# Optimization experiments

Measured on AMD Instinct MI355X. Metric: run time of the kernel, lower is better.

The kernel has to match this reference:

```python
import jax, jax.numpy as jnp
import numpy as np

DELTA = 0.1
LRELU_SLOPE = 0.01
BN_EPS = 1e-5


def ternarize(t, d):
    # {-1, 0, +1}: 0 where |t| < d, sign(t) otherwise (matches the torch where-chain)
    return jnp.where(jnp.abs(t) < d, 0.0, jnp.sign(t))


def ste_ternarize(t, d):
    # straight-through estimator, matching the torch .data-swap trick
    return t + jax.lax.stop_gradient(ternarize(t, d) - t)


def conv2d(x, w, stride, pad):
    return jax.lax.conv_general_dilated(
        x, w, (stride, stride), [(pad, pad), (pad, pad)],
        dimension_numbers=('NCHW', 'OIHW', 'NCHW'))


def batchnorm(x, gamma, beta, mean, var):
    inv = gamma / jnp.sqrt(var + BN_EPS)
    return x * inv[None, :, None, None] + (beta - mean * inv)[None, :, None, None]


def lrelu(x):
    return jnp.where(x > 0, x, LRELU_SLOPE * x)


def setup_inputs() -> dict:
    key = jax.random.key(0)
    ks = jax.random.split(key, 12)
    B, Cin, C, H, W = 16, 32, 64, 256, 256
    return {
        'x':      jax.random.normal(ks[0], (B, Cin, H, W), jnp.float32),
        'w11':    jax.random.normal(ks[1], (C, Cin, 3, 3), jnp.float32),
        'b11':    jax.random.normal(ks[2], (C,), jnp.float32),
        'w1':     jax.random.normal(ks[3], (C, Cin, 3, 3), jnp.float32),
        'b1':     jax.random.normal(ks[4], (C,), jnp.float32),
        'w2':     jax.random.normal(ks[5], (C, C, 3, 3), jnp.float32),
        'b2':     jax.random.normal(ks[6], (C,), jnp.float32),
        'gamma_p': jax.random.uniform(ks[7], (Cin,), jnp.float32),
        'beta_p':  jax.random.normal(ks[8], (Cin,), jnp.float32),
        'mean_p':  jax.random.normal(ks[9], (Cin,), jnp.float32),
        'var_p':   jnp.ones((Cin,), jnp.float32),
        'gamma1':  jax.random.uniform(ks[10], (C,), jnp.float32),
        'beta1':   jax.random.normal(ks[11], (C,), jnp.float32),
        'mean1':   jax.random.normal(jax.random.fold_in(key, 99), (C,), jnp.float32),
        'var1':    jnp.ones((C,), jnp.float32),
    }


def reference(x, w11, b11, w1, b1, w2, b2,
              gamma_p, beta_p, mean_p, var_p,
              gamma1, beta1, mean1, var1):
    # shortcut conv11 (stride 3); NOTE: torch mutates input.data in-place, so
    # the main branch below consumes the x already ternarized with d11.
    d11 = DELTA * jnp.max(jnp.abs(w11))
    x_t = ste_ternarize(x, d11)
    prev_mp = conv2d(x_t, ste_ternarize(w11, d11), 3, 1) \
        + ste_ternarize(b11, d11)[None, :, None, None]

    # main branch: pre_bn -> lrelu -> conv1 (stride 1) -> bn1 -> lrelu -> dropout(eval) -> conv2 (stride 3)
    out = lrelu(batchnorm(x_t, gamma_p, beta_p, mean_p, var_p))

    d1 = DELTA * jnp.max(jnp.abs(w1))
    out = conv2d(ste_ternarize(out, d1), ste_ternarize(w1, d1), 1, 1) \
        + ste_ternarize(b1, d1)[None, :, None, None]
    out = lrelu(batchnorm(out, gamma1, beta1, mean1, var1))
    # dropout: identity in eval mode

    d2 = DELTA * jnp.max(jnp.abs(w2))
    out = conv2d(ste_ternarize(out, d2), ste_ternarize(w2, d2), 3, 1) \
        + ste_ternarize(b2, d2)[None, :, None, None]

    return lrelu(out + prev_mp)  # [16, 64, 86, 86]
```

## Files before the change

### kernel.cpp

```cpp
#include <hip/hip_runtime.h>
#include <stdint.h>

#define B 16
#define CIN 32
#define C 64
#define H 256
#define W 256
#define OH 86
#define OW 86
#define PIX (OH*OW)
#define PADW 272
#define PWORDS (PADW*PADW*8)

typedef int v4i __attribute__((ext_vector_type(4)));

#define OFF_D      0
#define OFF_MAPW   64
#define OFF_B11    768
#define OFF_B2     1280
#define OFF_TLO    1536
#define OFF_THI    1792
#define OFF_W11R   4096
#define OFF_W1R    24576
#define OFF_W2R    45056
#define OFF_XTP    262144
#define OFF_XMAP   38141952

__device__ __forceinline__ int tern_i(float t, float d) {
    return (fabsf(t) < d) ? 0 : (t > 0.f ? 1 : -1);
}

__global__ __launch_bounds__(256) void k_pad(char* ws) {
    int idx = blockIdx.x * 256 + threadIdx.x;
    if (blockIdx.x == 0 && threadIdx.x < 3)
        ((unsigned*)(ws + OFF_D))[threadIdx.x] = 0u;
    if (idx >= 135168) return;
    int n = idx / 8448, c = idx - n * 8448;
    int row, col;
    if (c < 4352) {
        int r = c / 272; col = c - r * 272; row = (r < 2) ? r : r + 256;
    } else {
        int c2 = c - 4352; int k = c2 & 15;
        row = 2 + (c2 >> 4); col = (k < 2) ? k : k + 256;
    }
    size_t base = ((size_t)n * (PADW * PADW) + (size_t)row * PADW + col) * 2;
    int4 z = make_int4(0, 0, 0, 0);
    ((int4*)(ws + OFF_XTP))[base] = z;  ((int4*)(ws + OFF_XTP))[base + 1] = z;
    ((int4*)(ws + OFF_XMAP))[base] = z; ((int4*)(ws + OFF_XMAP))[base + 1] = z;
}

__global__ __launch_bounds__(256) void k_absmax(const float* w11, const float* w1,
                                                const float* w2, unsigned* dws) {
    __shared__ unsigned red[256];
    int b = blockIdx.x >> 4, sub = blockIdx.x & 15;
    const float* p = (b == 0) ? w11 : (b == 1) ? w1 : w2;
    int n = (b == 2) ? 36864 : 18432;
    int chunk = (n + 15) >> 4;
    int lo = sub * chunk, hi = min(lo + chunk, n);
    unsigned m = 0;
    for (int i = lo + threadIdx.x; i < hi; i += 256)
        m = max(m, __float_as_uint(fabsf(p[i])));
    red[threadIdx.x] = m; __syncthreads();
    for (int s = 128; s > 0; s >>= 1) {
        if (threadIdx.x < s) red[threadIdx.x] = max(red[threadIdx.x], red[threadIdx.x + s]);
        __syncthreads();
    }
    if (threadIdx.x == 0) atomicMax(&dws[b], red[0]);
}

__global__ __launch_bounds__(256) void k_prep(const float* w11, const float* w1, const float* w2,
                                              const float* b11, const float* b1, const float* b2,
                                              const float* gp, const float* bp, const float* mp, const float* vp,
                                              const float* g1, const float* be1, const float* me1, const float* v1,
                                              char* ws) {
    const unsigned* dw = (const unsigned*)(ws + OFF_D);
    float d11 = __fmul_rn(0.1f, __uint_as_float(dw[0]));
    float d1  = __fmul_rn(0.1f, __uint_as_float(dw[1]));
    float d2v = __fmul_rn(0.1f, __uint_as_float(dw[2]));
    int idx = blockIdx.x * 256 + threadIdx.x;
    if (idx < 4608) {
        int j = idx & 3, c16 = (idx >> 2) & 15, cot = (idx >> 6) & 3;
        int q1 = (idx >> 8) & 1, pos = idx >> 9;
        int co = cot * 16 + c16;
        unsigned wd = 0;
        #pragma unroll
        for (int jj = 0; jj < 4; jj++) {
            int ci = q1 * 16 + j * 4 + jj;
            int tv = tern_i(w1[(co * 32 + ci) * 9 + pos], d1);
            wd |= ((unsigned)(tv & 255)) << (8 * jj);
        }
        ((int*)(ws + OFF_W1R))[idx] = (int)wd;
    } else if (idx < 9216) {
        int i2 = idx - 4608;
        int j = i2 & 3, c16 = (i2 >> 2) & 15, cot = (i2 >> 6) & 3;
        int q1 = (i2 >> 8) & 1, pos = i2 >> 9;
        int co = cot * 16 + c16;
        unsigned wd = 0;
        #pragma unroll
        for (int jj = 0; jj < 4; jj++) {
            int ci = q1 * 16 + j * 4 + jj;
            int tv = tern_i(w11[(co * 32 + ci) * 9 + pos], d11);
            wd |= ((unsigned)(tv & 255)) << (8 * jj);
        }
        ((int*)(ws + OFF_W11R))[i2] = (int)wd;
    } else if (idx < 18432) {
        int i2 = idx - 9216;
        int j = i2 & 3, q = (i2 >> 2) & 3, c16 = (i2 >> 4) & 15;
        int cot = (i2 >> 8) & 3, pos = i2 >> 10;
        int co = cot * 16 + c16;
        unsigned wd = 0;
        #pragma unroll
        for (int jj = 0; jj < 4; jj++) {
            int ci = q * 16 + j * 4 + jj;
            int tv = tern_i(w2[(co * 64 + ci) * 9 + pos], d2v);
            wd |= ((unsigned)(tv & 255)) << (8 * jj);
        }
        ((int*)(ws + OFF_W2R))[i2] = (int)wd;
    } else {
        int i = idx - 18432;
        if (i < 64) {
            ((int*)(ws + OFF_B11))[i] = tern_i(b11[i], d11);
        } else if (i < 128) {
            ((int*)(ws + OFF_B2))[i - 64] = tern_i(b2[i - 64], d2v);
        } else if (i < 152) {
            int j = i - 128;
            int g = j / 3, s = j % 3;
            float v = (float)(s - 1);
            unsigned wd = 0;
            #pragma unroll
            for (int jj = 0; jj < 4; jj++) {
                int c = g * 4 + jj;
                float inv = __fdiv_rn(gp[c], __fsqrt_rn(__fadd_rn(vp[c], 1e-5f)));
                float sh  = __fsub_rn(bp[c], __fmul_rn(mp[c], inv));
                float z   = __fadd_rn(__fmul_rn(v, inv), sh);
                z = (z > 0.f) ? z : __fmul_rn(0.01f, z);
                wd |= ((unsigned)(tern_i(z, d1) & 255)) << (8 * jj);
            }
            ((int*)(ws + OFF_MAPW))[j] = (int)wd;
        } else if (i < 216) {
            int co = i - 152;
            float inv = __fdiv_rn(g1[co], __fsqrt_rn(__fadd_rn(v1[co], 1e-5f)));
            float sh  = __fsub_rn(be1[co], __fmul_rn(me1[co], inv));
            int lo = 1000, hi = 1000;
            for (int vi = -290; vi <= 290; ++vi) {
                float z = __fadd_rn(__fmul_rn((float)vi, inv), sh);
                z = (z > 0.f) ? z : __fmul_rn(0.01f, z);
                int cls = (fabsf(z) < d2v) ? 0 : (z > 0.f ? 1 : -1);
                if (cls >= 0 && lo == 1000) lo = vi;
                if (cls == 1 && hi == 1000) hi = vi;
            }
            int b1t = tern_i(b1[co], d1);
            ((int*)(ws + OFF_TLO))[co] = lo - b1t;
            ((int*)(ws + OFF_THI))[co] = hi - b1t;
        }
    }
}

__global__ __launch_bounds__(256) void k_tern_x(const float* __restrict__ x,
                                                char* __restrict__ ws) {
    float d11 = __fmul_rn(0.1f, __uint_as_float(((const unsigned*)(ws + OFF_D))[0]));
    const int* mapw = (const int*)(ws + OFF_MAPW);
    int idx = blockIdx.x * 256 + threadIdx.x;
    int pix = idx & 65535, n = idx >> 16;
    int y = pix >> 8, xq = pix & 255;
    const float* xp = x + ((size_t)n * CIN << 16) + pix;
    int rw[8], mw[8];
    #pragma unroll
    for (int g = 0; g < 8; ++g) {
        unsigned r = 0, m = 0;
        #pragma unroll
        for (int j = 0; j < 4; ++j) {
            float v = xp[(size_t)(g * 4 + j) << 16];
            int tv = tern_i(v, d11);
            r |= ((unsigned)(tv & 255)) << (8 * j);
            m |= (((unsigned)mapw[g * 3 + tv + 1] >> (8 * j)) & 255u) << (8 * j);
        }
        rw[g] = (int)r; mw[g] = (int)m;
    }
    size_t base = ((size_t)n * (PADW * PADW) + (size_t)(y + 2) * PADW + (xq + 2)) * 2;
    int4* o1 = (int4*)(ws + OFF_XTP) + base;
    o1[0] = make_int4(rw[0], rw[1], rw[2], rw[3]);
    o1[1] = make_int4(rw[4], rw[5], rw[6], rw[7]);
    int4* o2 = (int4*)(ws + OFF_XMAP) + base;
    o2[0] = make_int4(mw[0], mw[1], mw[2], mw[3]);
    o2[1] = make_int4(mw[4], mw[5], mw[6], mw[7]);
}

__global__ __launch_bounds__(256, 4) void k_net(const char* __restrict__ ws,
                                                float* __restrict__ out) {
    __shared__ int t2L[576 * 16];
    int tid = threadIdx.x, bid = blockIdx.x;
    int tx = bid % 11; int tt = bid / 11; int ty = tt % 11; int n = tt / 11;
    int OH0 = ty * 8, OW0 = tx * 8;
    int Y0 = OH0 * 3 - 2, X0 = OW0 * 3 - 2;
    int c16 = tid & 15, q = (tid >> 4) & 3, wv = tid >> 6;
    int q1 = q & 1, qh = q >> 1;
    const int* xmapn = (const int*)(ws + OFF_XMAP) + (size_t)n * PWORDS;
    const int* xtpn  = (const int*)(ws + OFF_XTP)  + (size_t)n * PWORDS;

    const int* w1r = (const int*)(ws + OFF_W1R);
    v4i bw1[5][4];
    #pragma unroll
    for (int c = 0; c < 5; ++c) {
        int pos = 2 * c + qh;
        #pragma unroll
        for (int ct = 0; ct < 4; ++ct) {
            v4i z = {0, 0, 0, 0};
            if (pos < 9) z = *(const v4i*)&w1r[((pos * 2 + q1) * 4 + ct) * 64 + c16 * 4];
            bw1[c][ct] = z;
        }
    }
    const int* TLO = (const int*)(ws + OFF_TLO);
    const int* THI = (const int*)(ws + OFF_THI);
    int tlo[4], thi[4];
    #pragma unroll
    for (int ct = 0; ct < 4; ++ct) { tlo[ct] = TLO[ct * 16 + c16]; thi[ct] = THI[ct * 16 + c16]; }

    int Yb = Y0 + 2, Xb = X0 + 2;
    #pragma unroll 1
    for (int pg = 0; pg < 9; ++pg) {
        int pbase = (wv * 9 + pg) * 16;
        int fp = pbase + c16;
        int iy = fp / 24, ix = fp - iy * 24;
        v4i a[5];
        #pragma unroll
        for (int c = 0; c < 5; ++c) {
            int pos = 2 * c + qh;
            v4i z = {0, 0, 0, 0};
            if (pos < 9) {
                int kh = pos / 3, kw = pos - kh * 3;
                z = *(const v4i*)&xmapn[((Yb + iy + kh) * PADW + (Xb + ix + kw)) * 8 + q1 * 4];
            }
            a[c] = z;
        }
        int pwr = pbase + q * 4 + (c16 & 3);
        int wy = pwr / 24, wx = pwr - wy * 24;
        bool wok = ((unsigned)(Y0 + 1 + wy) < H) && ((unsigned)(X0 + 1 + wx) < W);
        int wsw = (pwr >> 1) & 3;
        #pragma unroll
        for (int ct = 0; ct < 4; ++ct) {
            v4i acc = {0, 0, 0, 0};
            #pragma unroll
            for (int c = 0; c < 5; ++c)
                acc = __builtin_amdgcn_mfma_i32_16x16x64_i8(a[c], bw1[c][ct], acc, 0, 0, 0);
            unsigned wcol = 0;
            #pragma unroll
            for (int i = 0; i < 4; ++i) {
                int cls = (acc[i] >= tlo[ct] ? 1 : 0) + (acc[i] >= thi[ct] ? 1 : 0) - 1;
                wcol |= ((unsigned)(cls & 255)) << (8 * i);
            }
            unsigned y1 = (unsigned)__shfl_xor((int)wcol, 1);
            unsigned z1 = ((c16 & 1) == 0)
                        ? __builtin_amdgcn_perm(y1, wcol, 0x06020400u)
                        : __builtin_amdgcn_perm(y1, wcol, 0x03070105u);
            unsigned y2 = (unsigned)__shfl_xor((int)z1, 2);
            unsigned r  = ((c16 & 2) == 0)
                        ? __builtin_amdgcn_perm(y2, z1, 0x05040100u)
                        : __builtin_amdgcn_perm(y2, z1, 0x03020706u);
            t2L[pwr * 16 + (ct ^ wsw) * 4 + (c16 >> 2)] = wok ? (int)r : 0;
        }
    }
    __syncthreads();

    int o = wv * 16 + c16;
    int oh8 = o >> 3, ow8 = o & 7;
    int gOH = OH0 + oh8, gOW = OW0 + ow8;
    v4i a11[5];
    #pragma unroll
    for (int c = 0; c < 5; ++c) {
        int pos = 2 * c + qh;
        v4i z = {0, 0, 0, 0};
        if (pos < 9) {
            int kh = pos / 3, kw = pos - kh * 3;
            int ih = gOH * 3 - 1 + kh, iw = gOW * 3 - 1 + kw;
            z = *(const v4i*)&xtpn[((ih + 2) * PADW + (iw + 2)) * 8 + q1 * 4];
        }
        a11[c] = z;
    }
    v4i a2[9];
    #pragma unroll
    for (int pos = 0; pos < 9; ++pos) {
        int kh = pos / 3, kw = pos - kh * 3;
        int p2 = (oh8 * 3 + kh) * 24 + ow8 * 3 + kw;
        int g2 = q ^ ((p2 >> 1) & 3);
        a2[pos] = *(const v4i*)&t2L[p2 * 16 + g2 * 4];
    }
    const int* w2r = (const int*)(ws + OFF_W2R);
    const int* w11r = (const int*)(ws + OFF_W11R);
    v4i acc2[4], acc11[4];
    #pragma unroll
    for (int ct = 0; ct < 4; ++ct) {
        v4i acc = {0, 0, 0, 0};
        #pragma unroll
        for (int pos = 0; pos < 9; ++pos) {
            v4i b = *(const v4i*)&w2r[((pos * 4 + ct) * 16 + c16) * 16 + q * 4];
            acc = __builtin_amdgcn_mfma_i32_16x16x64_i8(a2[pos], b, acc, 0, 0, 0);
        }
        acc2[ct] = acc;
        v4i acc1 = {0, 0, 0, 0};
        #pragma unroll
        for (int c = 0; c < 5; ++c) {
            int pos = 2 * c + qh;
            v4i b = {0, 0, 0, 0};
            if (pos < 9) b = *(const v4i*)&w11r[((pos * 2 + q1) * 4 + ct) * 64 + c16 * 4];
            acc1 = __builtin_amdgcn_mfma_i32_16x16x64_i8(a11[c], b, acc1, 0, 0, 0);
        }
        acc11[ct] = acc1;
    }

    const int* b2i = (const int*)(ws + OFF_B2);
    const int* b11i = (const int*)(ws + OFF_B11);
    int pt0 = wv * 16 + q * 4;
    int ohh = OH0 + (pt0 >> 3);
    int oww = OW0 + (pt0 & 7);
    if (ohh < OH) {
        #pragma unroll
        for (int ct = 0; ct < 4; ++ct) {
            int co = ct * 16 + c16;
            int bc = b2i[co] + b11i[co];
            float f[4];
            #pragma unroll
            for (int i = 0; i < 4; ++i) {
                float z = (float)(acc2[ct][i] + acc11[ct][i] + bc);
                f[i] = (z > 0.f) ? z : __fmul_rn(0.01f, z);
            }
            float* op = out + ((size_t)(n * 64 + co)) * PIX + ohh * OW + oww;
            if (oww + 3 < OW) {
                *(float4*)op = make_float4(f[0], f[1], f[2], f[3]);
            } else {
                #pragma unroll
                for (int i = 0; i < 4; ++i)
                    if (oww + i < OW) op[i] = f[i];
            }
        }
    }
}

extern "C" void kernel_launch(void* const* d_in, const int* in_sizes, int n_in,
                              void* d_out, int out_size, void* d_ws, size_t ws_size,
                              hipStream_t stream) {
    const float* x    = (const float*)d_in[0];
    const float* w11  = (const float*)d_in[1];
    const float* b11  = (const float*)d_in[2];
    const float* w1   = (const float*)d_in[3];
    const float* b1   = (const float*)d_in[4];
    const float* w2   = (const float*)d_in[5];
    const float* b2   = (const float*)d_in[6];
    const float* gp   = (const float*)d_in[7];
    const float* bp   = (const float*)d_in[8];
    const float* mp   = (const float*)d_in[9];
    const float* vp   = (const float*)d_in[10];
    const float* g1   = (const float*)d_in[11];
    const float* be1  = (const float*)d_in[12];
    const float* me1  = (const float*)d_in[13];
    const float* v1   = (const float*)d_in[14];
    char* ws = (char*)d_ws;
    float* out = (float*)d_out;

    k_pad<<<528, 256, 0, stream>>>(ws);
    k_absmax<<<48, 256, 0, stream>>>(w11, w1, w2, (unsigned*)(ws + OFF_D));
    k_prep<<<73, 256, 0, stream>>>(w11, w1, w2, b11, b1, b2,
                                   gp, bp, mp, vp, g1, be1, me1, v1, ws);
    k_tern_x<<<4096, 256, 0, stream>>>(x, ws);
    k_net<<<11 * 11 * B, 256, 0, stream>>>(ws, out);
}
```

Measured before the change: 154.9 us.

## Prefetch next conv1 input tile and move shortcut conv before barrier

Software-pipelines the conv1 loop by loading the next pixel group's A operands while MFMAs for the current group run, hiding global load latency. The shortcut conv11 MFMAs are moved ahead of the __syncthreads so they overlap the barrier wait rather than following it. Launch bounds drop from 4 to 3 blocks per CU to make room for the extra prefetch registers, which risks lower occupancy.

```diff
diff --git a/kernel.cpp b/kernel.cpp
--- a/kernel.cpp
+++ b/kernel.cpp
@@ -186,7 +186,7 @@
     o2[1] = make_int4(mw[4], mw[5], mw[6], mw[7]);
 }
 
-__global__ __launch_bounds__(256, 4) void k_net(const char* __restrict__ ws,
+__global__ __launch_bounds__(256, 3) void k_net(const char* __restrict__ ws,
                                                 float* __restrict__ out) {
     __shared__ int t2L[576 * 16];
     int tid = threadIdx.x, bid = blockIdx.x;
@@ -217,12 +217,10 @@
     for (int ct = 0; ct < 4; ++ct) { tlo[ct] = TLO[ct * 16 + c16]; thi[ct] = THI[ct * 16 + c16]; }
 
     int Yb = Y0 + 2, Xb = X0 + 2;
-    #pragma unroll 1
-    for (int pg = 0; pg < 9; ++pg) {
-        int pbase = (wv * 9 + pg) * 16;
-        int fp = pbase + c16;
+    v4i aC[5];
+    {
+        int fp = wv * 144 + c16;
         int iy = fp / 24, ix = fp - iy * 24;
-        v4i a[5];
         #pragma unroll
         for (int c = 0; c < 5; ++c) {
             int pos = 2 * c + qh;
@@ -231,8 +229,26 @@
                 int kh = pos / 3, kw = pos - kh * 3;
                 z = *(const v4i*)&xmapn[((Yb + iy + kh) * PADW + (Xb + ix + kw)) * 8 + q1 * 4];
             }
-            a[c] = z;
-        }
+            aC[c] = z;
+        }
+    }
+    #pragma unroll 1
+    for (int pg = 0; pg < 9; ++pg) {
+        int pgn = (pg < 8) ? pg + 1 : 8;
+        int fpn = (wv * 9 + pgn) * 16 + c16;
+        int iyn = fpn / 24, ixn = fpn - iyn * 24;
+        v4i aN[5];
+        #pragma unroll
+        for (int c = 0; c < 5; ++c) {
+            int pos = 2 * c + qh;
+            v4i z = {0, 0, 0, 0};
+            if (pos < 9) {
+                int kh = pos / 3, kw = pos - kh * 3;
+                z = *(const v4i*)&xmapn[((Yb + iyn + kh) * PADW + (Xb + ixn + kw)) * 8 + q1 * 4];
+            }
+            aN[c] = z;
+        }
+        int pbase = (wv * 9 + pg) * 16;
         int pwr = pbase + q * 4 + (c16 & 3);
         int wy = pwr / 24, wx = pwr - wy * 24;
         bool wok = ((unsigned)(Y0 + 1 + wy) < H) && ((unsigned)(X0 + 1 + wx) < W);
@@ -242,7 +258,7 @@
             v4i acc = {0, 0, 0, 0};
             #pragma unroll
             for (int c = 0; c < 5; ++c)
-                acc = __builtin_amdgcn_mfma_i32_16x16x64_i8(a[c], bw1[c][ct], acc, 0, 0, 0);
+                acc = __builtin_amdgcn_mfma_i32_16x16x64_i8(aC[c], bw1[c][ct], acc, 0, 0, 0);
             unsigned wcol = 0;
             #pragma unroll
             for (int i = 0; i < 4; ++i) {
@@ -259,8 +275,9 @@
                         : __builtin_amdgcn_perm(y2, z1, 0x03020706u);
             t2L[pwr * 16 + (ct ^ wsw) * 4 + (c16 >> 2)] = wok ? (int)r : 0;
         }
-    }
-    __syncthreads();
+        #pragma unroll
+        for (int c = 0; c < 5; ++c) aC[c] = aN[c];
+    }
 
     int o = wv * 16 + c16;
     int oh8 = o >> 3, ow8 = o & 7;
@@ -277,6 +294,22 @@
         }
         a11[c] = z;
     }
+    const int* w11r = (const int*)(ws + OFF_W11R);
+    v4i acc11[4];
+    #pragma unroll
+    for (int ct = 0; ct < 4; ++ct) {
+        v4i acc1 = {0, 0, 0, 0};
+        #pragma unroll
+        for (int c = 0; c < 5; ++c) {
+            int pos = 2 * c + qh;
+            v4i b = {0, 0, 0, 0};
+            if (pos < 9) b = *(const v4i*)&w11r[((pos * 2 + q1) * 4 + ct) * 64 + c16 * 4];
+            acc1 = __builtin_amdgcn_mfma_i32_16x16x64_i8(a11[c], b, acc1, 0, 0, 0);
+        }
+        acc11[ct] = acc1;
+    }
+    __syncthreads();
+
     v4i a2[9];
     #pragma unroll
     for (int pos = 0; pos < 9; ++pos) {
@@ -286,8 +319,7 @@
         a2[pos] = *(const v4i*)&t2L[p2 * 16 + g2 * 4];
     }
     const int* w2r = (const int*)(ws + OFF_W2R);
-    const int* w11r = (const int*)(ws + OFF_W11R);
-    v4i acc2[4], acc11[4];
+    v4i acc2[4];
     #pragma unroll
     for (int ct = 0; ct < 4; ++ct) {
         v4i acc = {0, 0, 0, 0};
@@ -297,15 +329,6 @@
             acc = __builtin_amdgcn_mfma_i32_16x16x64_i8(a2[pos], b, acc, 0, 0, 0);
         }
         acc2[ct] = acc;
-        v4i acc1 = {0, 0, 0, 0};
-        #pragma unroll
-        for (int c = 0; c < 5; ++c) {
-            int pos = 2 * c + qh;
-            v4i b = {0, 0, 0, 0};
-            if (pos < 9) b = *(const v4i*)&w11r[((pos * 2 + q1) * 4 + ct) * 64 + c16 * 4];
-            acc1 = __builtin_amdgcn_mfma_i32_16x16x64_i8(a11[c], b, acc1, 0, 0, 0);
-        }
-        acc11[ct] = acc1;
     }
 
     const int* b2i = (const int*)(ws + OFF_B2);
```

Result: faster. 143.8 us (-7.2%).

## Fold padding into ternarize kernel, swap MFMA operands, hoist shortcut conv before barrier

Applied to the files above, without the earlier changes.

The border-padding writes move into extra blocks of the ternarize kernel, leaving only a tiny kernel to zero the absmax words. In the conv1 stage the MFMA operands are swapped so each lane's accumulator already holds packed channel bytes, which removes the two-step shuffle/perm transpose. Thresholds are now loaded per output row. The stride-3 shortcut conv is computed before the LDS barrier so it can overlap with other waves finishing conv1. Launch bounds drop to 3 waves per SIMD, which gives more registers but lowers occupancy.

```diff
diff --git a/kernel.cpp b/kernel.cpp
--- a/kernel.cpp
+++ b/kernel.cpp
@@ -30,23 +30,8 @@
     return (fabsf(t) < d) ? 0 : (t > 0.f ? 1 : -1);
 }
 
-__global__ __launch_bounds__(256) void k_pad(char* ws) {
-    int idx = blockIdx.x * 256 + threadIdx.x;
-    if (blockIdx.x == 0 && threadIdx.x < 3)
-        ((unsigned*)(ws + OFF_D))[threadIdx.x] = 0u;
-    if (idx >= 135168) return;
-    int n = idx / 8448, c = idx - n * 8448;
-    int row, col;
-    if (c < 4352) {
-        int r = c / 272; col = c - r * 272; row = (r < 2) ? r : r + 256;
-    } else {
-        int c2 = c - 4352; int k = c2 & 15;
-        row = 2 + (c2 >> 4); col = (k < 2) ? k : k + 256;
-    }
-    size_t base = ((size_t)n * (PADW * PADW) + (size_t)row * PADW + col) * 2;
-    int4 z = make_int4(0, 0, 0, 0);
-    ((int4*)(ws + OFF_XTP))[base] = z;  ((int4*)(ws + OFF_XTP))[base + 1] = z;
-    ((int4*)(ws + OFF_XMAP))[base] = z; ((int4*)(ws + OFF_XMAP))[base + 1] = z;
+__global__ void k_zero(unsigned* d) {
+    if (threadIdx.x < 3) d[threadIdx.x] = 0u;
 }
 
 __global__ __launch_bounds__(256) void k_absmax(const float* w11, const float* w1,
@@ -158,9 +143,26 @@
 
 __global__ __launch_bounds__(256) void k_tern_x(const float* __restrict__ x,
                                                 char* __restrict__ ws) {
+    int bidx = blockIdx.x;
+    if (bidx >= 4096) {
+        int idx = (bidx - 4096) * 256 + threadIdx.x;
+        int n = idx / 8448, c = idx - n * 8448;
+        int row, col;
+        if (c < 4352) {
+            int r = c / 272; col = c - r * 272; row = (r < 2) ? r : r + 256;
+        } else {
+            int c2 = c - 4352; int k = c2 & 15;
+            row = 2 + (c2 >> 4); col = (k < 2) ? k : k + 256;
+        }
+        size_t base = ((size_t)n * (PADW * PADW) + (size_t)row * PADW + col) * 2;
+        int4 z = make_int4(0, 0, 0, 0);
+        ((int4*)(ws + OFF_XTP))[base] = z;  ((int4*)(ws + OFF_XTP))[base + 1] = z;
+        ((int4*)(ws + OFF_XMAP))[base] = z; ((int4*)(ws + OFF_XMAP))[base + 1] = z;
+        return;
+    }
     float d11 = __fmul_rn(0.1f, __uint_as_float(((const unsigned*)(ws + OFF_D))[0]));
     const int* mapw = (const int*)(ws + OFF_MAPW);
-    int idx = blockIdx.x * 256 + threadIdx.x;
+    int idx = bidx * 256 + threadIdx.x;
     int pix = idx & 65535, n = idx >> 16;
     int y = pix >> 8, xq = pix & 255;
     const float* xp = x + ((size_t)n * CIN << 16) + pix;
@@ -186,7 +188,7 @@
     o2[1] = make_int4(mw[4], mw[5], mw[6], mw[7]);
 }
 
-__global__ __launch_bounds__(256, 4) void k_net(const char* __restrict__ ws,
+__global__ __launch_bounds__(256, 3) void k_net(const char* __restrict__ ws,
                                                 float* __restrict__ out) {
     __shared__ int t2L[576 * 16];
     int tid = threadIdx.x, bid = blockIdx.x;
@@ -212,9 +214,12 @@
     }
     const int* TLO = (const int*)(ws + OFF_TLO);
     const int* THI = (const int*)(ws + OFF_THI);
-    int tlo[4], thi[4];
-    #pragma unroll
-    for (int ct = 0; ct < 4; ++ct) { tlo[ct] = TLO[ct * 16 + c16]; thi[ct] = THI[ct * 16 + c16]; }
+    v4i tlo4[4], thi4[4];
+    #pragma unroll
+    for (int ct = 0; ct < 4; ++ct) {
+        tlo4[ct] = *(const v4i*)&TLO[ct * 16 + q * 4];
+        thi4[ct] = *(const v4i*)&THI[ct * 16 + q * 4];
+    }
 
     int Yb = Y0 + 2, Xb = X0 + 2;
     #pragma unroll 1
@@ -233,34 +238,23 @@
             }
             a[c] = z;
         }
-        int pwr = pbase + q * 4 + (c16 & 3);
-        int wy = pwr / 24, wx = pwr - wy * 24;
-        bool wok = ((unsigned)(Y0 + 1 + wy) < H) && ((unsigned)(X0 + 1 + wx) < W);
-        int wsw = (pwr >> 1) & 3;
+        bool wok = ((unsigned)(Y0 + 1 + iy) < H) && ((unsigned)(X0 + 1 + ix) < W);
+        int key = (fp >> 1) & 3;
         #pragma unroll
         for (int ct = 0; ct < 4; ++ct) {
             v4i acc = {0, 0, 0, 0};
             #pragma unroll
             for (int c = 0; c < 5; ++c)
-                acc = __builtin_amdgcn_mfma_i32_16x16x64_i8(a[c], bw1[c][ct], acc, 0, 0, 0);
+                acc = __builtin_amdgcn_mfma_i32_16x16x64_i8(bw1[c][ct], a[c], acc, 0, 0, 0);
             unsigned wcol = 0;
             #pragma unroll
             for (int i = 0; i < 4; ++i) {
-                int cls = (acc[i] >= tlo[ct] ? 1 : 0) + (acc[i] >= thi[ct] ? 1 : 0) - 1;
+                int cls = (acc[i] >= tlo4[ct][i] ? 1 : 0) + (acc[i] >= thi4[ct][i] ? 1 : 0) - 1;
                 wcol |= ((unsigned)(cls & 255)) << (8 * i);
             }
-            unsigned y1 = (unsigned)__shfl_xor((int)wcol, 1);
-            unsigned z1 = ((c16 & 1) == 0)
-                        ? __builtin_amdgcn_perm(y1, wcol, 0x06020400u)
-                        : __builtin_amdgcn_perm(y1, wcol, 0x03070105u);
-            unsigned y2 = (unsigned)__shfl_xor((int)z1, 2);
-            unsigned r  = ((c16 & 2) == 0)
-                        ? __builtin_amdgcn_perm(y2, z1, 0x05040100u)
-                        : __builtin_amdgcn_perm(y2, z1, 0x03020706u);
-            t2L[pwr * 16 + (ct ^ wsw) * 4 + (c16 >> 2)] = wok ? (int)r : 0;
-        }
-    }
-    __syncthreads();
+            t2L[fp * 16 + ((ct ^ key) << 2) + q] = wok ? (int)wcol : 0;
+        }
+    }
 
     int o = wv * 16 + c16;
     int oh8 = o >> 3, ow8 = o & 7;
@@ -277,6 +271,22 @@
         }
         a11[c] = z;
     }
+    const int* w11r = (const int*)(ws + OFF_W11R);
+    v4i acc11[4];
+    #pragma unroll
+    for (int ct = 0; ct < 4; ++ct) {
+        v4i acc1 = {0, 0, 0, 0};
+        #pragma unroll
+        for (int c = 0; c < 5; ++c) {
+            int pos = 2 * c + qh;
+            v4i b = {0, 0, 0, 0};
+            if (pos < 9) b = *(const v4i*)&w11r[((pos * 2 + q1) * 4 + ct) * 64 + c16 * 4];
+            acc1 = __builtin_amdgcn_mfma_i32_16x16x64_i8(a11[c], b, acc1, 0, 0, 0);
+        }
+        acc11[ct] = acc1;
+    }
+    __syncthreads();
+
     v4i a2[9];
     #pragma unroll
     for (int pos = 0; pos < 9; ++pos) {
@@ -286,8 +296,7 @@
         a2[pos] = *(const v4i*)&t2L[p2 * 16 + g2 * 4];
     }
     const int* w2r = (const int*)(ws + OFF_W2R);
-    const int* w11r = (const int*)(ws + OFF_W11R);
-    v4i acc2[4], acc11[4];
+    v4i acc2[4];
     #pragma unroll
     for (int ct = 0; ct < 4; ++ct) {
         v4i acc = {0, 0, 0, 0};
@@ -297,15 +306,6 @@
             acc = __builtin_amdgcn_mfma_i32_16x16x64_i8(a2[pos], b, acc, 0, 0, 0);
         }
         acc2[ct] = acc;
-        v4i acc1 = {0, 0, 0, 0};
-        #pragma unroll
-        for (int c = 0; c < 5; ++c) {
-            int pos = 2 * c + qh;
-            v4i b = {0, 0, 0, 0};
-            if (pos < 9) b = *(const v4i*)&w11r[((pos * 2 + q1) * 4 + ct) * 64 + c16 * 4];
-            acc1 = __builtin_amdgcn_mfma_i32_16x16x64_i8(a11[c], b, acc1, 0, 0, 0);
-        }
-        acc11[ct] = acc1;
     }
 
     const int* b2i = (const int*)(ws + OFF_B2);
@@ -357,10 +357,10 @@
     char* ws = (char*)d_ws;
     float* out = (float*)d_out;
 
-    k_pad<<<528, 256, 0, stream>>>(ws);
+    k_zero<<<1, 64, 0, stream>>>((unsigned*)(ws + OFF_D));
     k_absmax<<<48, 256, 0, stream>>>(w11, w1, w2, (unsigned*)(ws + OFF_D));
     k_prep<<<73, 256, 0, stream>>>(w11, w1, w2, b11, b1, b2,
                                    gp, bp, mp, vp, g1, be1, me1, v1, ws);
-    k_tern_x<<<4096, 256, 0, stream>>>(x, ws);
+    k_tern_x<<<4096 + 528, 256, 0, stream>>>(x, ws);
     k_net<<<11 * 11 * B, 256, 0, stream>>>(ws, out);
 }
```

After: 140.0 us. -9.6%, faster.
